# Kernel tuning notes

Measured on AMD Instinct MI355X. Metric: run time of the kernel, lower is better.

## Reference

```python
import jax, jax.numpy as jnp
import numpy as np
import math

NUM_HEADS = 16  # power of two -> simple ALiBi slope formula

def alibi_slopes(num_heads: int) -> jnp.ndarray:
    # num_heads is a power of two here; general formula per Press et al. 2022
    k = 1 << (num_heads.bit_length() - 1)
    ratio = 2.0 ** (-8.0 / k)
    slopes = ratio ** np.arange(1, 1 + k)
    if num_heads != k:
        ratio2 = 2.0 ** (-8.0 / (2 * k))
        rest = (ratio2 ** np.arange(1, 1 + 2 * k, 2))[: num_heads - k]
        slopes = np.concatenate([slopes, rest])
    return jnp.asarray(slopes, dtype=jnp.float32).reshape(1, -1, 1, 1)


def setup_inputs() -> dict:
    key = jax.random.key(0)
    kq, kk, kv, km = jax.random.split(key, 4)
    B, H, S, D = 1, NUM_HEADS, 2048, 64
    query = jax.random.normal(kq, (B, H, S, D), dtype=jnp.float32)
    k_ = jax.random.normal(kk, (B, H, S, D), dtype=jnp.float32)
    value = jax.random.normal(kv, (B, H, S, D), dtype=jnp.float32)
    # padding-style boolean mask [B, S]; keep position 0 always valid
    mask = jax.random.randint(km, (B, S), 0, 2).astype(bool)
    mask = mask.at[:, 0].set(True)
    return {"query": query, "key": k_, "value": value, "mask": mask}


def reference(query, key, value, mask):
    B, H, S, D = query.shape
    scale = 1.0 / math.sqrt(D)
    # scores: [B, H, Sq, Sk]
    scores = jnp.einsum("bhqd,bhkd->bhqk", query, key) * scale
    # causal ALiBi bias: distances arange(1-S, 1) -> shape (1, H, 1, S)
    distances = jnp.arange(1 - S, 1, dtype=jnp.float32)
    bias = distances[None, None, None, :] * alibi_slopes(H)
    scores = scores + bias
    # boolean padding mask [B, S] -> [B, 1, 1, S]
    blocked = jnp.finfo(scores.dtype).min
    scores = jnp.where(mask[:, None, None, :], scores, blocked)
    weights = jax.nn.softmax(scores, axis=-1)
    # dropout_prob = 0.0 (eval) -> identity
    return jnp.einsum("bhqk,bhkd->bhqd", weights, value)
```

## Files before the change

### kernel.cpp

```cpp
#include <hip/hip_runtime.h>


constexpr int   S_LEN  = 2048;
constexpr int   D_DIM  = 64;
constexpr int   H_NUM  = 16;
constexpr int   QT     = 128;
constexpr int   K_TILE = 64;
constexpr int   NTILE  = S_LEN / K_TILE;
constexpr int   MAXNC  = 8;
constexpr int   QB     = S_LEN / QT;
constexpr int   PROWSTR= 36;
constexpr float SCL    = 0.18033688f;
constexpr float L2E    = 1.44269504f;
constexpr float MASKED = -50000.0f;
constexpr float CUTOFF = 40.0f;

typedef short bf16x8 __attribute__((ext_vector_type(8)));
typedef short bf16x4 __attribute__((ext_vector_type(4)));
typedef float f32x4  __attribute__((ext_vector_type(4)));

__device__ inline short f2bf(float f) {
    union { float f; unsigned u; } x; x.f = f;
    return (short)((x.u + 0x7fffu + ((x.u >> 16) & 1u)) >> 16);
}

__device__ inline unsigned pack2bf(float a, float b) {
#if __has_builtin(__builtin_amdgcn_cvt_pk_bf16_f32)
    auto p = __builtin_amdgcn_cvt_pk_bf16_f32(a, b);
    unsigned u; __builtin_memcpy(&u, &p, 4); return u;
#else
    return (unsigned)(unsigned short)f2bf(a) | ((unsigned)(unsigned short)f2bf(b) << 16);
#endif
}

__device__ inline float fexp2(float x) {
#if __has_builtin(__builtin_amdgcn_exp2f)
    return __builtin_amdgcn_exp2f(x);
#else
    return exp2f(x);
#endif
}

__device__ inline unsigned permb(unsigned hi, unsigned lo, unsigned sel) {
#if __has_builtin(__builtin_amdgcn_perm)
    return __builtin_amdgcn_perm(hi, lo, sel);
#else
    return (sel == 0x05040100u) ? ((lo & 0xffffu) | (hi << 16))
                                : ((lo >> 16) | (hi & 0xffff0000u));
#endif
}

__device__ inline void load_lds16(const void* g, void* l) {
    __builtin_amdgcn_global_load_lds((const __attribute__((address_space(1))) void*)g,
                                     (__attribute__((address_space(3))) void*)l, 16, 0, 0);
}

__device__ inline int head_t0(int h) {
    const float slope_l2e = exp2f(-0.5f * (float)(h + 1)) * L2E;
    const float kmin = 2047.0f - CUTOFF / slope_l2e;
    return kmin <= 0.0f ? 0 : ((int)kmin) >> 6;
}
__device__ inline int head_nc(int h) {
    const int nt = NTILE - head_t0(h);
    const int nc = (nt + 3) >> 2;
    return nc > MAXNC ? MAXNC : nc;
}

__global__ __launch_bounds__(256)
void preprocess_kernel(const float* __restrict__ Km, const float* __restrict__ Vm,
                       const void* __restrict__ maskp,
                       short* __restrict__ Kswz, short* __restrict__ Vswz,
                       float* __restrict__ Bias)
{
    __shared__ int mask_is_i32;
    const int tid = threadIdx.x;
    const int kt = blockIdx.x, h = blockIdx.y;
    if (kt < head_t0(h)) return;

    const int kbase = kt * K_TILE;
    const size_t tbase = ((size_t)h * S_LEN + kbase) * D_DIM;
    short* Kd = Kswz + ((size_t)h * NTILE + kt) * 4096;
    short* Vd = Vswz + ((size_t)h * NTILE + kt) * 4096;

    if (tid < 64) {
        const unsigned v = ((const unsigned*)maskp)[tid];
        const unsigned long long b = __ballot(v <= 1u);
        if (tid == 0) mask_is_i32 = (b == ~0ULL);
    }

    #pragma unroll
    for (int it = 0; it < 2; ++it) {
        const int idx = it * 256 + tid;
        const int key = idx >> 3, c = idx & 7;
        const float* src = Km + tbase + key * 64 + c * 8;
        float4 a = *(const float4*)src;
        float4 b = *(const float4*)(src + 4);
        unsigned u[4] = { pack2bf(a.x, a.y), pack2bf(a.z, a.w),
                          pack2bf(b.x, b.y), pack2bf(b.z, b.w) };
        bf16x8 kp; __builtin_memcpy(&kp, u, 16);
        *(bf16x8*)(Kd + key * 64 + ((c ^ (key & 7)) << 3)) = kp;
    }

    {
        const int db = tid >> 4, kb = tid & 15;
        const int d4 = db * 4, key4 = kb * 4;
        float4 vv[4];
        #pragma unroll
        for (int j = 0; j < 4; ++j)
            vv[j] = *(const float4*)(Vm + tbase + (key4 + j) * 64 + d4);
        const float* vp = (const float*)vv;
        #pragma unroll
        for (int jj = 0; jj < 4; ++jj) {
            const int d = d4 + jj;
            bf16x4 ov;
            ov[0] = f2bf(vp[0 * 4 + jj]); ov[1] = f2bf(vp[1 * 4 + jj]);
            ov[2] = f2bf(vp[2 * 4 + jj]); ov[3] = f2bf(vp[3 * 4 + jj]);
            *(bf16x4*)(Vd + d * 64 + (((key4 >> 3) ^ (d & 7)) << 3) + (key4 & 7)) = ov;
        }
    }
    __syncthreads();
    if (tid < K_TILE) {
        const int key = kbase + tid;
        const int mv = mask_is_i32 ? ((const int*)maskp)[key]
                                   : (int)((const unsigned char*)maskp)[key];
        const float slope_l2e = exp2f(-0.5f * (float)(h + 1)) * L2E;
        Bias[h * S_LEN + key] = mv ? slope_l2e * (float)(key - (S_LEN - 1)) : MASKED;
    }
}

__global__ __launch_bounds__(256, 4)
void attn_main(const float* __restrict__ Qm, const short* __restrict__ Kswz,
               const short* __restrict__ Vswz, const float* __restrict__ Bias,
               float* __restrict__ Om, float* __restrict__ Opart,
               float* __restrict__ lp)
{
    __shared__ short    k_lds[4096];
    __shared__ short    v_lds[4096];
    __shared__ float    bm_lds[64];
    __shared__ unsigned p_lds[4][32 * PROWSTR];

    const int tid = threadIdx.x;
    const int wave = tid >> 6, lane = tid & 63;
    const int l16 = lane & 15, quad = lane >> 4;
    const int h = blockIdx.y, qblk = blockIdx.x, c = blockIdx.z;

    const int nc = head_nc(h);
    if (c >= nc) return;
    const int t0 = head_t0(h);
    const int nt = NTILE - t0;
    const int tstart = t0 + (c * nt) / nc;
    const int tend   = t0 + ((c + 1) * nt) / nc;

    const unsigned psel = (quad < 2) ? 0x05040100u : 0x07060302u;

    bf16x8 qfrag[2][2];
    {
        const float* Qh = Qm + (size_t)h * S_LEN * D_DIM;
        #pragma unroll
        for (int s = 0; s < 2; ++s) {
            const int qrow = qblk * QT + wave * 32 + s * 16 + l16;
            #pragma unroll
            for (int t = 0; t < 2; ++t) {
                const float* src = Qh + (size_t)qrow * D_DIM + t * 32 + quad * 8;
                float4 a = *(const float4*)src;
                float4 b = *(const float4*)(src + 4);
                unsigned* qp = (unsigned*)&qfrag[s][t];
                qp[0] = pack2bf(a.x * SCL, a.y * SCL);
                qp[1] = pack2bf(a.z * SCL, a.w * SCL);
                qp[2] = pack2bf(b.x * SCL, b.y * SCL);
                qp[3] = pack2bf(b.z * SCL, b.w * SCL);
            }
        }
    }

    bf16x8 onesv;
    #pragma unroll
    for (int i = 0; i < 8; ++i) onesv[i] = (short)0x3F80;

    f32x4 o_frag[2][4], l4[2];
    #pragma unroll
    for (int s = 0; s < 2; ++s) {
        #pragma unroll
        for (int cc = 0; cc < 4; ++cc) o_frag[s][cc] = (f32x4){0.f, 0.f, 0.f, 0.f};
        l4[s] = (f32x4){0.f, 0.f, 0.f, 0.f};
    }

    const short* Kh = Kswz + (size_t)h * NTILE * 4096;
    const short* Vh = Vswz + (size_t)h * NTILE * 4096;
    const float* Bh = Bias + h * S_LEN;
    unsigned* pw = p_lds[wave];
    const int swz = l16 & 7;

    for (int kt = tstart; kt < tend; ++kt) {
        __syncthreads();
        {
            const char* kg = (const char*)(Kh + (size_t)kt * 4096);
            const char* vg = (const char*)(Vh + (size_t)kt * 4096);
            char* kl = (char*)k_lds + wave * 2048;
            char* vl = (char*)v_lds + wave * 2048;
            const int go = wave * 2048 + lane * 16;
            load_lds16(kg + go,        kl);
            load_lds16(kg + go + 1024, kl + 1024);
            load_lds16(vg + go,        vl);
            load_lds16(vg + go + 1024, vl + 1024);
        }
        if (tid < 16) {
            float4 b4 = *(const float4*)(Bh + kt * K_TILE + tid * 4);
            *(float4*)&bm_lds[tid * 4] = b4;
        }
        __syncthreads();

        f32x4 sv[2][4];
        #pragma unroll
        for (int cc = 0; cc < 4; ++cc) {
            const float b = bm_lds[cc * 16 + l16];
            const f32x4 binit = (f32x4){b, b, b, b};
            sv[0][cc] = binit;
            sv[1][cc] = binit;
            #pragma unroll
            for (int t = 0; t < 2; ++t) {
                bf16x8 bfrag = *(const bf16x8*)&k_lds[(cc * 16 + l16) * 64 + (((t * 4 + quad) ^ swz) << 3)];
                sv[0][cc] = __builtin_amdgcn_mfma_f32_16x16x32_bf16(qfrag[0][t], bfrag, sv[0][cc], 0, 0, 0);
                sv[1][cc] = __builtin_amdgcn_mfma_f32_16x16x32_bf16(qfrag[1][t], bfrag, sv[1][cc], 0, 0, 0);
            }
        }

        #pragma unroll
        for (int s = 0; s < 2; ++s) {
            #pragma unroll
            for (int r = 0; r < 4; ++r) {
                const float p0 = fexp2(sv[s][0][r]);
                const float p1 = fexp2(sv[s][1][r]);
                const float p2 = fexp2(sv[s][2][r]);
                const float p3 = fexp2(sv[s][3][r]);
                unsigned* pp = &pw[(s * 16 + quad * 4 + r) * PROWSTR + l16];
                pp[0]  = pack2bf(p0, p1);
                pp[16] = pack2bf(p2, p3);
            }
        }

        #pragma unroll
        for (int t2 = 0; t2 < 2; ++t2) {
            bf16x8 pfrag[2];
            #pragma unroll
            for (int s = 0; s < 2; ++s) {
                const unsigned* pr = &pw[(s * 16 + l16) * PROWSTR + t2 * 16 + (quad & 1) * 8];
                uint4 w0 = *(const uint4*)(pr);
                uint4 w1 = *(const uint4*)(pr + 4);
                unsigned pf[4];
                pf[0] = permb(w0.y, w0.x, psel);
                pf[1] = permb(w0.w, w0.z, psel);
                pf[2] = permb(w1.y, w1.x, psel);
                pf[3] = permb(w1.w, w1.z, psel);
                __builtin_memcpy(&pfrag[s], pf, 16);
            }
            #pragma unroll
            for (int c2 = 0; c2 < 4; ++c2) {
                bf16x8 vfrag = *(const bf16x8*)&v_lds[(c2 * 16 + l16) * 64 + (((t2 * 4 + quad) ^ swz) << 3)];
                o_frag[0][c2] = __builtin_amdgcn_mfma_f32_16x16x32_bf16(pfrag[0], vfrag, o_frag[0][c2], 0, 0, 0);
                o_frag[1][c2] = __builtin_amdgcn_mfma_f32_16x16x32_bf16(pfrag[1], vfrag, o_frag[1][c2], 0, 0, 0);
            }
            l4[0] = __builtin_amdgcn_mfma_f32_16x16x32_bf16(pfrag[0], onesv, l4[0], 0, 0, 0);
            l4[1] = __builtin_amdgcn_mfma_f32_16x16x32_bf16(pfrag[1], onesv, l4[1], 0, 0, 0);
        }
    }

    if (nc == 1) {
        float* Oh = Om + (size_t)h * S_LEN * D_DIM;
        const int qrow0 = qblk * QT + wave * 32;
        #pragma unroll
        for (int s = 0; s < 2; ++s) {
            #pragma unroll
            for (int r = 0; r < 4; ++r) {
                const float inv = 1.0f / l4[s][r];
                const int row = qrow0 + s * 16 + quad * 4 + r;
                float* dst = Oh + (size_t)row * D_DIM + l16;
                dst[0]  = o_frag[s][0][r] * inv;
                dst[16] = o_frag[s][1][r] * inv;
                dst[32] = o_frag[s][2][r] * inv;
                dst[48] = o_frag[s][3][r] * inv;
            }
        }
    } else {
        #pragma unroll
        for (int s = 0; s < 2; ++s) {
            const int g = qblk * 32 + wave * 8 + s * 4 + quad;
            const size_t gbase = (((size_t)h * MAXNC + c) * 512 + g);
            #pragma unroll
            for (int c2 = 0; c2 < 4; ++c2) {
                float* dst = Opart + (gbase * 64 + c2 * 16 + l16) * 4;
                *(f32x4*)dst = o_frag[s][c2];
            }
            if (l16 == 0) *(f32x4*)(lp + gbase * 4) = l4[s];
        }
    }
}

__global__ __launch_bounds__(256)
void attn_combine_kernel(const float* __restrict__ Opart, const float* __restrict__ lp,
                         float* __restrict__ Om)
{
    const int t   = blockIdx.x * 256 + threadIdx.x;
    const int col = t & 63;
    const int g   = (t >> 6) & 511;
    const int h   = t >> 15;

    const int nc = head_nc(h);
    if (nc == 1) return;

    f32x4 acc = (f32x4){0.f, 0.f, 0.f, 0.f};
    f32x4 den = (f32x4){0.f, 0.f, 0.f, 0.f};
    for (int c = 0; c < nc; ++c) {
        const size_t gbase = (((size_t)h * MAXNC + c) * 512 + g);
        den += *(const f32x4*)(lp + gbase * 4);
        acc += *(const f32x4*)(Opart + (gbase * 64 + col) * 4);
    }
    float* Oh = Om + (size_t)h * S_LEN * D_DIM;
    #pragma unroll
    for (int r = 0; r < 4; ++r)
        Oh[(size_t)(g * 4 + r) * 64 + col] = acc[r] / den[r];
}

extern "C" void kernel_launch(void* const* d_in, const int* in_sizes, int n_in,
                              void* d_out, int out_size, void* d_ws, size_t ws_size,
                              hipStream_t stream) {
    (void)in_sizes; (void)n_in; (void)out_size; (void)ws_size;
    const float* Q = (const float*)d_in[0];
    const float* K = (const float*)d_in[1];
    const float* V = (const float*)d_in[2];
    const void*  M = d_in[3];
    float* O = (float*)d_out;

    char* ws = (char*)d_ws;
    size_t off = 0;
    short* Kswz = (short*)(ws + off); off += (size_t)H_NUM * S_LEN * D_DIM * 2;
    short* Vswz = (short*)(ws + off); off += (size_t)H_NUM * S_LEN * D_DIM * 2;
    float* Bias = (float*)(ws + off); off += (size_t)H_NUM * S_LEN * 4;
    float* Opart = (float*)(ws + off); off += (size_t)H_NUM * MAXNC * 512 * 64 * 4 * 4;
    float* lp   = (float*)(ws + off); off += (size_t)H_NUM * MAXNC * 512 * 4 * 4;

    preprocess_kernel<<<dim3(NTILE, H_NUM), 256, 0, stream>>>(K, V, M, Kswz, Vswz, Bias);
    attn_main<<<dim3(QB, H_NUM, MAXNC), 256, 0, stream>>>(Q, Kswz, Vswz, Bias, O, Opart, lp);
    attn_combine_kernel<<<(H_NUM * 512 * 64) / 256, 256, 0, stream>>>(Opart, lp, O);
}
```

Baseline: 98.82 us.

## Fuse split-K combine into attention kernel via last-block atomic ticket

Removes the separate combine kernel. Each split block writes its partial output and row sums, increments a per-(head, q-block) atomic ticket, and the last-arriving block adds the other splits' partials into its registers, normalizes, and writes the final output. Tickets are zeroed in the preprocess kernel. This saves one kernel launch and its extra pass over the partial buffers, at the cost of threadfences, an atomic per block, and a serialized tail reduction in the last block.

```diff
diff --git a/kernel.cpp b/kernel.cpp
--- a/kernel.cpp
+++ b/kernel.cpp
@@ -70,11 +70,14 @@
 void preprocess_kernel(const float* __restrict__ Km, const float* __restrict__ Vm,
                        const void* __restrict__ maskp,
                        short* __restrict__ Kswz, short* __restrict__ Vswz,
-                       float* __restrict__ Bias)
+                       float* __restrict__ Bias, unsigned* __restrict__ Tickets)
 {
     __shared__ int mask_is_i32;
     const int tid = threadIdx.x;
     const int kt = blockIdx.x, h = blockIdx.y;
+
+    if (kt == 0 && tid < QB) Tickets[h * QB + tid] = 0u;
+
     if (kt < head_t0(h)) return;
 
     const int kbase = kt * K_TILE;
@@ -132,12 +135,13 @@
 void attn_main(const float* __restrict__ Qm, const short* __restrict__ Kswz,
                const short* __restrict__ Vswz, const float* __restrict__ Bias,
                float* __restrict__ Om, float* __restrict__ Opart,
-               float* __restrict__ lp)
+               float* __restrict__ lp, unsigned* __restrict__ Tickets)
 {
     __shared__ short    k_lds[4096];
     __shared__ short    v_lds[4096];
     __shared__ float    bm_lds[64];
     __shared__ unsigned p_lds[4][32 * PROWSTR];
+    __shared__ int      is_last;
 
     const int tid = threadIdx.x;
     const int wave = tid >> 6, lane = tid & 63;
@@ -293,32 +297,44 @@
             }
             if (l16 == 0) *(f32x4*)(lp + gbase * 4) = l4[s];
         }
-    }
-}
-
-__global__ __launch_bounds__(256)
-void attn_combine_kernel(const float* __restrict__ Opart, const float* __restrict__ lp,
-                         float* __restrict__ Om)
-{
-    const int t   = blockIdx.x * 256 + threadIdx.x;
-    const int col = t & 63;
-    const int g   = (t >> 6) & 511;
-    const int h   = t >> 15;
-
-    const int nc = head_nc(h);
-    if (nc == 1) return;
-
-    f32x4 acc = (f32x4){0.f, 0.f, 0.f, 0.f};
-    f32x4 den = (f32x4){0.f, 0.f, 0.f, 0.f};
-    for (int c = 0; c < nc; ++c) {
-        const size_t gbase = (((size_t)h * MAXNC + c) * 512 + g);
-        den += *(const f32x4*)(lp + gbase * 4);
-        acc += *(const f32x4*)(Opart + (gbase * 64 + col) * 4);
-    }
-    float* Oh = Om + (size_t)h * S_LEN * D_DIM;
-    #pragma unroll
-    for (int r = 0; r < 4; ++r)
-        Oh[(size_t)(g * 4 + r) * 64 + col] = acc[r] / den[r];
+
+        __threadfence();
+        if (tid == 0) {
+            const unsigned old = atomicAdd(&Tickets[h * QB + qblk], 1u);
+            is_last = (old == (unsigned)(nc - 1)) ? 1 : 0;
+        }
+        __syncthreads();
+        if (is_last) {
+            __threadfence();
+            #pragma unroll
+            for (int s = 0; s < 2; ++s) {
+                const int g = qblk * 32 + wave * 8 + s * 4 + quad;
+                for (int cc2 = 0; cc2 < nc; ++cc2) {
+                    if (cc2 == c) continue;
+                    const size_t gbase = (((size_t)h * MAXNC + cc2) * 512 + g);
+                    l4[s] += *(const f32x4*)(lp + gbase * 4);
+                    #pragma unroll
+                    for (int c2 = 0; c2 < 4; ++c2)
+                        o_frag[s][c2] += *(const f32x4*)(Opart + (gbase * 64 + c2 * 16 + l16) * 4);
+                }
+            }
+            float* Oh = Om + (size_t)h * S_LEN * D_DIM;
+            const int qrow0 = qblk * QT + wave * 32;
+            #pragma unroll
+            for (int s = 0; s < 2; ++s) {
+                #pragma unroll
+                for (int r = 0; r < 4; ++r) {
+                    const float inv = 1.0f / l4[s][r];
+                    const int row = qrow0 + s * 16 + quad * 4 + r;
+                    float* dst = Oh + (size_t)row * D_DIM + l16;
+                    dst[0]  = o_frag[s][0][r] * inv;
+                    dst[16] = o_frag[s][1][r] * inv;
+                    dst[32] = o_frag[s][2][r] * inv;
+                    dst[48] = o_frag[s][3][r] * inv;
+                }
+            }
+        }
+    }
 }
 
 extern "C" void kernel_launch(void* const* d_in, const int* in_sizes, int n_in,
@@ -338,8 +354,8 @@
     float* Bias = (float*)(ws + off); off += (size_t)H_NUM * S_LEN * 4;
     float* Opart = (float*)(ws + off); off += (size_t)H_NUM * MAXNC * 512 * 64 * 4 * 4;
     float* lp   = (float*)(ws + off); off += (size_t)H_NUM * MAXNC * 512 * 4 * 4;
-
-    preprocess_kernel<<<dim3(NTILE, H_NUM), 256, 0, stream>>>(K, V, M, Kswz, Vswz, Bias);
-    attn_main<<<dim3(QB, H_NUM, MAXNC), 256, 0, stream>>>(Q, Kswz, Vswz, Bias, O, Opart, lp);
-    attn_combine_kernel<<<(H_NUM * 512 * 64) / 256, 256, 0, stream>>>(Opart, lp, O);
-}
+    unsigned* Tickets = (unsigned*)(ws + off); off += (size_t)H_NUM * QB * 4;
+
+    preprocess_kernel<<<dim3(NTILE, H_NUM), 256, 0, stream>>>(K, V, M, Kswz, Vswz, Bias, Tickets);
+    attn_main<<<dim3(QB, H_NUM, MAXNC), 256, 0, stream>>>(Q, Kswz, Vswz, Bias, O, Opart, lp, Tickets);
+}
```

After: 222.4 us. +125.1%, slower.

## Replace split-K grid and combine kernel with intra-block two-way key split

Applied to the files above, without the earlier changes.

Drops the blockIdx.z split over key chunks and the separate combine kernel. Each 512-thread block now runs two groups of four waves that handle the two halves of a head's active key tiles, and merges their partial outputs and row sums through shared memory. K/V tiles are double-buffered in LDS with prefetch of the next tile, the whole bias row is staged once, and MFMA sections get raised scheduling priority. This removes one launch and the global partial-output traffic, but cuts grid parallelism on heads with long key ranges to two ways, which may leave CUs underused. Bias and K/V mean the split is no longer per-head adaptive.

```diff
diff --git a/kernel.cpp b/kernel.cpp
--- a/kernel.cpp
+++ b/kernel.cpp
@@ -7,7 +7,6 @@
 constexpr int   QT     = 128;
 constexpr int   K_TILE = 64;
 constexpr int   NTILE  = S_LEN / K_TILE;
-constexpr int   MAXNC  = 8;
 constexpr int   QB     = S_LEN / QT;
 constexpr int   PROWSTR= 36;
 constexpr float SCL    = 0.18033688f;
@@ -59,11 +58,6 @@
     const float slope_l2e = exp2f(-0.5f * (float)(h + 1)) * L2E;
     const float kmin = 2047.0f - CUTOFF / slope_l2e;
     return kmin <= 0.0f ? 0 : ((int)kmin) >> 6;
-}
-__device__ inline int head_nc(int h) {
-    const int nt = NTILE - head_t0(h);
-    const int nc = (nt + 3) >> 2;
-    return nc > MAXNC ? MAXNC : nc;
 }
 
 __global__ __launch_bounds__(256)
@@ -128,37 +122,57 @@
     }
 }
 
-__global__ __launch_bounds__(256, 4)
+__global__ __launch_bounds__(512, 2)
 void attn_main(const float* __restrict__ Qm, const short* __restrict__ Kswz,
                const short* __restrict__ Vswz, const float* __restrict__ Bias,
-               float* __restrict__ Om, float* __restrict__ Opart,
-               float* __restrict__ lp)
+               float* __restrict__ Om)
 {
-    __shared__ short    k_lds[4096];
-    __shared__ short    v_lds[4096];
-    __shared__ float    bm_lds[64];
-    __shared__ unsigned p_lds[4][32 * PROWSTR];
+    __shared__ short    k_lds[2][2][4096];
+    __shared__ short    v_lds[2][2][4096];
+    __shared__ float    bias_lds[S_LEN / QB * QB / 1];
+    __shared__ unsigned p_lds[8][32 * PROWSTR];
+    __shared__ float    l_cb[4][32];
+
+    static_assert(sizeof(bias_lds) == S_LEN * sizeof(float), "bias_lds size");
 
     const int tid = threadIdx.x;
     const int wave = tid >> 6, lane = tid & 63;
     const int l16 = lane & 15, quad = lane >> 4;
-    const int h = blockIdx.y, qblk = blockIdx.x, c = blockIdx.z;
-
-    const int nc = head_nc(h);
-    if (c >= nc) return;
+    const int sw = wave & 3;
+    const int cw = wave >> 2;
+    const int h = blockIdx.y, qblk = blockIdx.x;
+
     const int t0 = head_t0(h);
     const int nt = NTILE - t0;
-    const int tstart = t0 + (c * nt) / nc;
-    const int tend   = t0 + ((c + 1) * nt) / nc;
+    const int nhalf = (nt + 1) >> 1;
+    const int mylen  = (cw == 0) ? nhalf : nt - nhalf;
+    const int mybase = (cw == 0) ? t0 : t0 + nhalf;
 
     const unsigned psel = (quad < 2) ? 0x05040100u : 0x07060302u;
+    const short* Kh = Kswz + (size_t)h * NTILE * 4096;
+    const short* Vh = Vswz + (size_t)h * NTILE * 4096;
+    unsigned* pw = p_lds[wave];
+    const int swz = l16 & 7;
+    const int so  = sw * 2048 + lane * 16;
+
+    *(float4*)&bias_lds[tid * 4] = *(const float4*)(Bias + (size_t)h * S_LEN + tid * 4);
+    if (mylen > 0) {
+        const char* kg = (const char*)(Kh + (size_t)mybase * 4096);
+        const char* vg = (const char*)(Vh + (size_t)mybase * 4096);
+        char* kl = (char*)&k_lds[cw][0][0] + sw * 2048;
+        char* vl = (char*)&v_lds[cw][0][0] + sw * 2048;
+        load_lds16(kg + so,        kl);
+        load_lds16(kg + so + 1024, kl + 1024);
+        load_lds16(vg + so,        vl);
+        load_lds16(vg + so + 1024, vl + 1024);
+    }
 
     bf16x8 qfrag[2][2];
     {
         const float* Qh = Qm + (size_t)h * S_LEN * D_DIM;
         #pragma unroll
         for (int s = 0; s < 2; ++s) {
-            const int qrow = qblk * QT + wave * 32 + s * 16 + l16;
+            const int qrow = qblk * QT + sw * 32 + s * 16 + l16;
             #pragma unroll
             for (int t = 0; t < 2; ++t) {
                 const float* src = Qh + (size_t)qrow * D_DIM + t * 32 + quad * 8;
@@ -185,140 +199,126 @@
         l4[s] = (f32x4){0.f, 0.f, 0.f, 0.f};
     }
 
-    const short* Kh = Kswz + (size_t)h * NTILE * 4096;
-    const short* Vh = Vswz + (size_t)h * NTILE * 4096;
-    const float* Bh = Bias + h * S_LEN;
-    unsigned* pw = p_lds[wave];
-    const int swz = l16 & 7;
-
-    for (int kt = tstart; kt < tend; ++kt) {
+    __syncthreads();
+
+    for (int i = 0; i < nhalf; ++i) {
+        const int buf = i & 1;
+        if (i + 1 < mylen) {
+            const int ktn = mybase + i + 1;
+            const char* kg = (const char*)(Kh + (size_t)ktn * 4096);
+            const char* vg = (const char*)(Vh + (size_t)ktn * 4096);
+            char* kl = (char*)&k_lds[cw][buf ^ 1][0] + sw * 2048;
+            char* vl = (char*)&v_lds[cw][buf ^ 1][0] + sw * 2048;
+            load_lds16(kg + so,        kl);
+            load_lds16(kg + so + 1024, kl + 1024);
+            load_lds16(vg + so,        vl);
+            load_lds16(vg + so + 1024, vl + 1024);
+        }
+        if (i < mylen) {
+            const int kt = mybase + i;
+            const float* bm = &bias_lds[kt * K_TILE];
+            const short* kb = &k_lds[cw][buf][0];
+            const short* vb = &v_lds[cw][buf][0];
+
+            f32x4 sv[2][4];
+            __builtin_amdgcn_s_setprio(1);
+            #pragma unroll
+            for (int cc = 0; cc < 4; ++cc) {
+                const float b = bm[cc * 16 + l16];
+                const f32x4 binit = (f32x4){b, b, b, b};
+                sv[0][cc] = binit;
+                sv[1][cc] = binit;
+                #pragma unroll
+                for (int t = 0; t < 2; ++t) {
+                    bf16x8 bfrag = *(const bf16x8*)&kb[(cc * 16 + l16) * 64 + (((t * 4 + quad) ^ swz) << 3)];
+                    sv[0][cc] = __builtin_amdgcn_mfma_f32_16x16x32_bf16(qfrag[0][t], bfrag, sv[0][cc], 0, 0, 0);
+                    sv[1][cc] = __builtin_amdgcn_mfma_f32_16x16x32_bf16(qfrag[1][t], bfrag, sv[1][cc], 0, 0, 0);
+                }
+            }
+            __builtin_amdgcn_s_setprio(0);
+
+            #pragma unroll
+            for (int s = 0; s < 2; ++s) {
+                #pragma unroll
+                for (int r = 0; r < 4; ++r) {
+                    const float p0 = fexp2(sv[s][0][r]);
+                    const float p1 = fexp2(sv[s][1][r]);
+                    const float p2 = fexp2(sv[s][2][r]);
+                    const float p3 = fexp2(sv[s][3][r]);
+                    unsigned* pp = &pw[(s * 16 + quad * 4 + r) * PROWSTR + l16];
+                    pp[0]  = pack2bf(p0, p1);
+                    pp[16] = pack2bf(p2, p3);
+                }
+            }
+
+            #pragma unroll
+            for (int t2 = 0; t2 < 2; ++t2) {
+                bf16x8 pfrag[2];
+                #pragma unroll
+                for (int s = 0; s < 2; ++s) {
+                    const unsigned* pr = &pw[(s * 16 + l16) * PROWSTR + t2 * 16 + (quad & 1) * 8];
+                    uint4 w0 = *(const uint4*)(pr);
+                    uint4 w1 = *(const uint4*)(pr + 4);
+                    unsigned pf[4];
+                    pf[0] = permb(w0.y, w0.x, psel);
+                    pf[1] = permb(w0.w, w0.z, psel);
+                    pf[2] = permb(w1.y, w1.x, psel);
+                    pf[3] = permb(w1.w, w1.z, psel);
+                    __builtin_memcpy(&pfrag[s], pf, 16);
+                }
+                __builtin_amdgcn_s_setprio(1);
+                #pragma unroll
+                for (int c2 = 0; c2 < 4; ++c2) {
+                    bf16x8 vfrag = *(const bf16x8*)&vb[(c2 * 16 + l16) * 64 + (((t2 * 4 + quad) ^ swz) << 3)];
+                    o_frag[0][c2] = __builtin_amdgcn_mfma_f32_16x16x32_bf16(pfrag[0], vfrag, o_frag[0][c2], 0, 0, 0);
+                    o_frag[1][c2] = __builtin_amdgcn_mfma_f32_16x16x32_bf16(pfrag[1], vfrag, o_frag[1][c2], 0, 0, 0);
+                }
+                l4[0] = __builtin_amdgcn_mfma_f32_16x16x32_bf16(pfrag[0], onesv, l4[0], 0, 0, 0);
+                l4[1] = __builtin_amdgcn_mfma_f32_16x16x32_bf16(pfrag[1], onesv, l4[1], 0, 0, 0);
+                __builtin_amdgcn_s_setprio(0);
+            }
+        }
         __syncthreads();
-        {
-            const char* kg = (const char*)(Kh + (size_t)kt * 4096);
-            const char* vg = (const char*)(Vh + (size_t)kt * 4096);
-            char* kl = (char*)k_lds + wave * 2048;
-            char* vl = (char*)v_lds + wave * 2048;
-            const int go = wave * 2048 + lane * 16;
-            load_lds16(kg + go,        kl);
-            load_lds16(kg + go + 1024, kl + 1024);
-            load_lds16(vg + go,        vl);
-            load_lds16(vg + go + 1024, vl + 1024);
-        }
-        if (tid < 16) {
-            float4 b4 = *(const float4*)(Bh + kt * K_TILE + tid * 4);
-            *(float4*)&bm_lds[tid * 4] = b4;
-        }
-        __syncthreads();
-
-        f32x4 sv[2][4];
-        #pragma unroll
-        for (int cc = 0; cc < 4; ++cc) {
-            const float b = bm_lds[cc * 16 + l16];
-            const f32x4 binit = (f32x4){b, b, b, b};
-            sv[0][cc] = binit;
-            sv[1][cc] = binit;
-            #pragma unroll
-            for (int t = 0; t < 2; ++t) {
-                bf16x8 bfrag = *(const bf16x8*)&k_lds[(cc * 16 + l16) * 64 + (((t * 4 + quad) ^ swz) << 3)];
-                sv[0][cc] = __builtin_amdgcn_mfma_f32_16x16x32_bf16(qfrag[0][t], bfrag, sv[0][cc], 0, 0, 0);
-                sv[1][cc] = __builtin_amdgcn_mfma_f32_16x16x32_bf16(qfrag[1][t], bfrag, sv[1][cc], 0, 0, 0);
-            }
-        }
-
+    }
+
+    float* cb = (float*)p_lds;
+    if (cw == 1) {
         #pragma unroll
         for (int s = 0; s < 2; ++s) {
             #pragma unroll
+            for (int c2 = 0; c2 < 4; ++c2) {
+                #pragma unroll
+                for (int r = 0; r < 4; ++r)
+                    cb[(sw * 32 + s * 16 + quad * 4 + r) * 68 + c2 * 16 + l16] = o_frag[s][c2][r];
+            }
+            if (l16 == 0) {
+                #pragma unroll
+                for (int r = 0; r < 4; ++r)
+                    l_cb[sw][s * 16 + quad * 4 + r] = l4[s][r];
+            }
+        }
+    }
+    __syncthreads();
+    if (cw == 0) {
+        float* Oh = Om + (size_t)h * S_LEN * D_DIM;
+        const int qrow0 = qblk * QT + sw * 32;
+        #pragma unroll
+        for (int s = 0; s < 2; ++s) {
+            #pragma unroll
             for (int r = 0; r < 4; ++r) {
-                const float p0 = fexp2(sv[s][0][r]);
-                const float p1 = fexp2(sv[s][1][r]);
-                const float p2 = fexp2(sv[s][2][r]);
-                const float p3 = fexp2(sv[s][3][r]);
-                unsigned* pp = &pw[(s * 16 + quad * 4 + r) * PROWSTR + l16];
-                pp[0]  = pack2bf(p0, p1);
-                pp[16] = pack2bf(p2, p3);
-            }
-        }
-
-        #pragma unroll
-        for (int t2 = 0; t2 < 2; ++t2) {
-            bf16x8 pfrag[2];
-            #pragma unroll
-            for (int s = 0; s < 2; ++s) {
-                const unsigned* pr = &pw[(s * 16 + l16) * PROWSTR + t2 * 16 + (quad & 1) * 8];
-                uint4 w0 = *(const uint4*)(pr);
-                uint4 w1 = *(const uint4*)(pr + 4);
-                unsigned pf[4];
-                pf[0] = permb(w0.y, w0.x, psel);
-                pf[1] = permb(w0.w, w0.z, psel);
-                pf[2] = permb(w1.y, w1.x, psel);
-                pf[3] = permb(w1.w, w1.z, psel);
-                __builtin_memcpy(&pfrag[s], pf, 16);
-            }
-            #pragma unroll
-            for (int c2 = 0; c2 < 4; ++c2) {
-                bf16x8 vfrag = *(const bf16x8*)&v_lds[(c2 * 16 + l16) * 64 + (((t2 * 4 + quad) ^ swz) << 3)];
-                o_frag[0][c2] = __builtin_amdgcn_mfma_f32_16x16x32_bf16(pfrag[0], vfrag, o_frag[0][c2], 0, 0, 0);
-                o_frag[1][c2] = __builtin_amdgcn_mfma_f32_16x16x32_bf16(pfrag[1], vfrag, o_frag[1][c2], 0, 0, 0);
-            }
-            l4[0] = __builtin_amdgcn_mfma_f32_16x16x32_bf16(pfrag[0], onesv, l4[0], 0, 0, 0);
-            l4[1] = __builtin_amdgcn_mfma_f32_16x16x32_bf16(pfrag[1], onesv, l4[1], 0, 0, 0);
-        }
-    }
-
-    if (nc == 1) {
-        float* Oh = Om + (size_t)h * S_LEN * D_DIM;
-        const int qrow0 = qblk * QT + wave * 32;
-        #pragma unroll
-        for (int s = 0; s < 2; ++s) {
-            #pragma unroll
-            for (int r = 0; r < 4; ++r) {
-                const float inv = 1.0f / l4[s][r];
-                const int row = qrow0 + s * 16 + quad * 4 + r;
+                const int rrow = s * 16 + quad * 4 + r;
+                float lsum = l4[s][r] + l_cb[sw][rrow];
+                const float inv = 1.0f / lsum;
+                const int row = qrow0 + rrow;
                 float* dst = Oh + (size_t)row * D_DIM + l16;
-                dst[0]  = o_frag[s][0][r] * inv;
-                dst[16] = o_frag[s][1][r] * inv;
-                dst[32] = o_frag[s][2][r] * inv;
-                dst[48] = o_frag[s][3][r] * inv;
-            }
-        }
-    } else {
-        #pragma unroll
-        for (int s = 0; s < 2; ++s) {
-            const int g = qblk * 32 + wave * 8 + s * 4 + quad;
-            const size_t gbase = (((size_t)h * MAXNC + c) * 512 + g);
-            #pragma unroll
-            for (int c2 = 0; c2 < 4; ++c2) {
-                float* dst = Opart + (gbase * 64 + c2 * 16 + l16) * 4;
-                *(f32x4*)dst = o_frag[s][c2];
-            }
-            if (l16 == 0) *(f32x4*)(lp + gbase * 4) = l4[s];
-        }
-    }
-}
-
-__global__ __launch_bounds__(256)
-void attn_combine_kernel(const float* __restrict__ Opart, const float* __restrict__ lp,
-                         float* __restrict__ Om)
-{
-    const int t   = blockIdx.x * 256 + threadIdx.x;
-    const int col = t & 63;
-    const int g   = (t >> 6) & 511;
-    const int h   = t >> 15;
-
-    const int nc = head_nc(h);
-    if (nc == 1) return;
-
-    f32x4 acc = (f32x4){0.f, 0.f, 0.f, 0.f};
-    f32x4 den = (f32x4){0.f, 0.f, 0.f, 0.f};
-    for (int c = 0; c < nc; ++c) {
-        const size_t gbase = (((size_t)h * MAXNC + c) * 512 + g);
-        den += *(const f32x4*)(lp + gbase * 4);
-        acc += *(const f32x4*)(Opart + (gbase * 64 + col) * 4);
-    }
-    float* Oh = Om + (size_t)h * S_LEN * D_DIM;
-    #pragma unroll
-    for (int r = 0; r < 4; ++r)
-        Oh[(size_t)(g * 4 + r) * 64 + col] = acc[r] / den[r];
+                const float* cr = &cb[(sw * 32 + rrow) * 68];
+                dst[0]  = (o_frag[s][0][r] + cr[0  + l16]) * inv;
+                dst[16] = (o_frag[s][1][r] + cr[16 + l16]) * inv;
+                dst[32] = (o_frag[s][2][r] + cr[32 + l16]) * inv;
+                dst[48] = (o_frag[s][3][r] + cr[48 + l16]) * inv;
+            }
+        }
+    }
 }
 
 extern "C" void kernel_launch(void* const* d_in, const int* in_sizes, int n_in,
@@ -336,10 +336,7 @@
     short* Kswz = (short*)(ws + off); off += (size_t)H_NUM * S_LEN * D_DIM * 2;
     short* Vswz = (short*)(ws + off); off += (size_t)H_NUM * S_LEN * D_DIM * 2;
     float* Bias = (float*)(ws + off); off += (size_t)H_NUM * S_LEN * 4;
-    float* Opart = (float*)(ws + off); off += (size_t)H_NUM * MAXNC * 512 * 64 * 4 * 4;
-    float* lp   = (float*)(ws + off); off += (size_t)H_NUM * MAXNC * 512 * 4 * 4;
 
     preprocess_kernel<<<dim3(NTILE, H_NUM), 256, 0, stream>>>(K, V, M, Kswz, Vswz, Bias);
-    attn_main<<<dim3(QB, H_NUM, MAXNC), 256, 0, stream>>>(Q, Kswz, Vswz, Bias, O, Opart, lp);
-    attn_combine_kernel<<<(H_NUM * 512 * 64) / 256, 256, 0, stream>>>(Opart, lp, O);
-}
+    attn_main<<<dim3(QB, H_NUM), 512, 0, stream>>>(Q, Kswz, Vswz, Bias, O);
+}
```

Result: slower. 109.0 us (+10.3%).

## Keep softmax P in registers via transposed MFMA and permlane shuffles, drop P LDS

Applied to the files above, without the earlier changes.

Swaps the MFMA operand order so the score tile comes out transposed, which lets each lane's exp2 results be repacked into the PV A-operand through v_permlane32_swap and ds_swizzle. That removes the per-wave P staging buffer in LDS and its write/read round trip. Bias for up to four tiles is preloaded once per block instead of per tile, the K/V global-to-LDS load offsets are reorganised, s_setprio is wrapped around the MFMA sections, and the occupancy hint is raised from 4 to 5. The risks are correctness of the lane permutation and of the bias preload, which only covers four tiles; with nc capped at 8 a chunk could need more, and there is extra register pressure.

```diff
diff --git a/kernel.cpp b/kernel.cpp
--- a/kernel.cpp
+++ b/kernel.cpp
@@ -9,7 +9,6 @@
 constexpr int   NTILE  = S_LEN / K_TILE;
 constexpr int   MAXNC  = 8;
 constexpr int   QB     = S_LEN / QT;
-constexpr int   PROWSTR= 36;
 constexpr float SCL    = 0.18033688f;
 constexpr float L2E    = 1.44269504f;
 constexpr float MASKED = -50000.0f;
@@ -38,15 +37,6 @@
     return __builtin_amdgcn_exp2f(x);
 #else
     return exp2f(x);
-#endif
-}
-
-__device__ inline unsigned permb(unsigned hi, unsigned lo, unsigned sel) {
-#if __has_builtin(__builtin_amdgcn_perm)
-    return __builtin_amdgcn_perm(hi, lo, sel);
-#else
-    return (sel == 0x05040100u) ? ((lo & 0xffffu) | (hi << 16))
-                                : ((lo >> 16) | (hi & 0xffff0000u));
 #endif
 }
 
@@ -128,16 +118,15 @@
     }
 }
 
-__global__ __launch_bounds__(256, 4)
+__global__ __launch_bounds__(256, 5)
 void attn_main(const float* __restrict__ Qm, const short* __restrict__ Kswz,
                const short* __restrict__ Vswz, const float* __restrict__ Bias,
                float* __restrict__ Om, float* __restrict__ Opart,
                float* __restrict__ lp)
 {
-    __shared__ short    k_lds[4096];
-    __shared__ short    v_lds[4096];
-    __shared__ float    bm_lds[64];
-    __shared__ unsigned p_lds[4][32 * PROWSTR];
+    __shared__ short k_lds[4096];
+    __shared__ short v_lds[4096];
+    __shared__ float bias_lds[256];
 
     const int tid = threadIdx.x;
     const int wave = tid >> 6, lane = tid & 63;
@@ -151,7 +140,15 @@
     const int tstart = t0 + (c * nt) / nc;
     const int tend   = t0 + ((c + 1) * nt) / nc;
 
-    const unsigned psel = (quad < 2) ? 0x05040100u : 0x07060302u;
+    const short* Kh = Kswz + (size_t)h * NTILE * 4096;
+    const short* Vh = Vswz + (size_t)h * NTILE * 4096;
+    const int swz = l16 & 7;
+
+    {
+        const int tt = tid >> 6;
+        if (tstart + tt < tend)
+            bias_lds[tid] = Bias[(size_t)h * S_LEN + (tstart + tt) * K_TILE + (tid & 63)];
+    }
 
     bf16x8 qfrag[2][2];
     {
@@ -185,57 +182,50 @@
         l4[s] = (f32x4){0.f, 0.f, 0.f, 0.f};
     }
 
-    const short* Kh = Kswz + (size_t)h * NTILE * 4096;
-    const short* Vh = Vswz + (size_t)h * NTILE * 4096;
-    const float* Bh = Bias + h * S_LEN;
-    unsigned* pw = p_lds[wave];
-    const int swz = l16 & 7;
-
     for (int kt = tstart; kt < tend; ++kt) {
         __syncthreads();
         {
             const char* kg = (const char*)(Kh + (size_t)kt * 4096);
             const char* vg = (const char*)(Vh + (size_t)kt * 4096);
-            char* kl = (char*)k_lds + wave * 2048;
-            char* vl = (char*)v_lds + wave * 2048;
-            const int go = wave * 2048 + lane * 16;
+            char* kl = (char*)k_lds + wave * 1024;
+            char* vl = (char*)v_lds + wave * 1024;
+            const int go = wave * 1024 + lane * 16;
             load_lds16(kg + go,        kl);
-            load_lds16(kg + go + 1024, kl + 1024);
+            load_lds16(kg + go + 4096, kl + 4096);
             load_lds16(vg + go,        vl);
-            load_lds16(vg + go + 1024, vl + 1024);
-        }
-        if (tid < 16) {
-            float4 b4 = *(const float4*)(Bh + kt * K_TILE + tid * 4);
-            *(float4*)&bm_lds[tid * 4] = b4;
+            load_lds16(vg + go + 4096, vl + 4096);
         }
         __syncthreads();
 
+        const float* bm = &bias_lds[(kt - tstart) * K_TILE];
+
         f32x4 sv[2][4];
+        __builtin_amdgcn_s_setprio(1);
         #pragma unroll
         for (int cc = 0; cc < 4; ++cc) {
-            const float b = bm_lds[cc * 16 + l16];
-            const f32x4 binit = (f32x4){b, b, b, b};
+            const f32x4 binit = *(const f32x4*)&bm[cc * 16 + quad * 4];
             sv[0][cc] = binit;
             sv[1][cc] = binit;
             #pragma unroll
             for (int t = 0; t < 2; ++t) {
-                bf16x8 bfrag = *(const bf16x8*)&k_lds[(cc * 16 + l16) * 64 + (((t * 4 + quad) ^ swz) << 3)];
-                sv[0][cc] = __builtin_amdgcn_mfma_f32_16x16x32_bf16(qfrag[0][t], bfrag, sv[0][cc], 0, 0, 0);
-                sv[1][cc] = __builtin_amdgcn_mfma_f32_16x16x32_bf16(qfrag[1][t], bfrag, sv[1][cc], 0, 0, 0);
-            }
-        }
-
+                bf16x8 kfrag = *(const bf16x8*)&k_lds[(cc * 16 + l16) * 64 + (((t * 4 + quad) ^ swz) << 3)];
+                sv[0][cc] = __builtin_amdgcn_mfma_f32_16x16x32_bf16(kfrag, qfrag[0][t], sv[0][cc], 0, 0, 0);
+                sv[1][cc] = __builtin_amdgcn_mfma_f32_16x16x32_bf16(kfrag, qfrag[1][t], sv[1][cc], 0, 0, 0);
+            }
+        }
+        __builtin_amdgcn_s_setprio(0);
+
+        unsigned pu[2][4][2];
         #pragma unroll
         for (int s = 0; s < 2; ++s) {
             #pragma unroll
-            for (int r = 0; r < 4; ++r) {
-                const float p0 = fexp2(sv[s][0][r]);
-                const float p1 = fexp2(sv[s][1][r]);
-                const float p2 = fexp2(sv[s][2][r]);
-                const float p3 = fexp2(sv[s][3][r]);
-                unsigned* pp = &pw[(s * 16 + quad * 4 + r) * PROWSTR + l16];
-                pp[0]  = pack2bf(p0, p1);
-                pp[16] = pack2bf(p2, p3);
+            for (int cc = 0; cc < 4; ++cc) {
+                const float p0 = fexp2(sv[s][cc][0]);
+                const float p1 = fexp2(sv[s][cc][1]);
+                const float p2 = fexp2(sv[s][cc][2]);
+                const float p3 = fexp2(sv[s][cc][3]);
+                pu[s][cc][0] = pack2bf(p0, p1);
+                pu[s][cc][1] = pack2bf(p2, p3);
             }
         }
 
@@ -244,16 +234,23 @@
             bf16x8 pfrag[2];
             #pragma unroll
             for (int s = 0; s < 2; ++s) {
-                const unsigned* pr = &pw[(s * 16 + l16) * PROWSTR + t2 * 16 + (quad & 1) * 8];
-                uint4 w0 = *(const uint4*)(pr);
-                uint4 w1 = *(const uint4*)(pr + 4);
+                unsigned a0 = pu[s][2 * t2][0],     a1 = pu[s][2 * t2][1];
+                unsigned b0 = pu[s][2 * t2 + 1][0], b1 = pu[s][2 * t2 + 1][1];
+                asm volatile("v_permlane32_swap_b32 %0, %1" : "+v"(a0), "+v"(b0));
+                asm volatile("v_permlane32_swap_b32 %0, %1" : "+v"(a1), "+v"(b1));
+                const unsigned sa0 = __builtin_amdgcn_ds_swizzle(a0, 0x401F);
+                const unsigned sa1 = __builtin_amdgcn_ds_swizzle(a1, 0x401F);
+                const unsigned sb0 = __builtin_amdgcn_ds_swizzle(b0, 0x401F);
+                const unsigned sb1 = __builtin_amdgcn_ds_swizzle(b1, 0x401F);
+                const bool hi = (quad & 1);
                 unsigned pf[4];
-                pf[0] = permb(w0.y, w0.x, psel);
-                pf[1] = permb(w0.w, w0.z, psel);
-                pf[2] = permb(w1.y, w1.x, psel);
-                pf[3] = permb(w1.w, w1.z, psel);
+                pf[0] = hi ? sb0 : a0;
+                pf[1] = hi ? sb1 : a1;
+                pf[2] = hi ? b0 : sa0;
+                pf[3] = hi ? b1 : sa1;
                 __builtin_memcpy(&pfrag[s], pf, 16);
             }
+            __builtin_amdgcn_s_setprio(1);
             #pragma unroll
             for (int c2 = 0; c2 < 4; ++c2) {
                 bf16x8 vfrag = *(const bf16x8*)&v_lds[(c2 * 16 + l16) * 64 + (((t2 * 4 + quad) ^ swz) << 3)];
@@ -262,6 +259,7 @@
             }
             l4[0] = __builtin_amdgcn_mfma_f32_16x16x32_bf16(pfrag[0], onesv, l4[0], 0, 0, 0);
             l4[1] = __builtin_amdgcn_mfma_f32_16x16x32_bf16(pfrag[1], onesv, l4[1], 0, 0, 0);
+            __builtin_amdgcn_s_setprio(0);
         }
     }
 
```

Measured after the change: 105.1 us. 6.3% more time.
